# Performance work log

Measured on AMD Instinct MI355X. Metric: run time of the kernel, lower is better.

The kernel has to match this reference:

```python
import jax, jax.numpy as jnp
import numpy as np

BIG = 1e11  # torch code replaces zero counts with 1e11 before dividing
N_LABELS = 5


def _label_mean(state, func):
    """Masked mean per label (1..5). state [..., S, H], func [..., S] int.
    Returns aug [..., 5, H], aug_mask [..., 5] bool. Zero-count labels -> 0
    (sum is exactly 0 and denom is BIG, matching the torch zero-init path)."""
    mask = (func[..., None] == jnp.arange(1, N_LABELS + 1)).astype(state.dtype)  # [...,S,5]
    sums = jnp.einsum('...sl,...sh->...lh', mask, state)                          # [...,5,H]
    counts = mask.sum(axis=-2)                                                    # [...,5]
    aug_mask = counts > 0
    denom = jnp.where(aug_mask, counts, jnp.asarray(BIG, state.dtype))
    return sums / denom[..., None], aug_mask


def _masked_mean(state, func):
    """Mean over all non-pad (func != 0) sentences. state [..., S, H]."""
    m = (func != 0).astype(state.dtype)
    s = jnp.einsum('...s,...sh->...h', m, state)
    c = m.sum(axis=-1)
    pm = c > 0
    denom = jnp.where(pm, c, jnp.asarray(BIG, state.dtype))
    return s / denom[..., None], pm


def setup_inputs() -> dict:
    key = jax.random.key(0)
    k1, k2, k3, k4 = jax.random.split(key, 4)
    B, TS, H = 8, 512, 512       # batch, tar_n_sents, enc_hidden_size
    D, RS = 32, 256              # ref_n_docs, ref_n_sents
    return {
        'tarsent_state': jax.random.normal(k1, (B, TS, H), jnp.float32),
        'tar_func': jax.random.randint(k2, (B, TS), 0, 6),
        'refsent_state': jax.random.normal(k3, (B, D, RS, H), jnp.float32),
        'ref_func': jax.random.randint(k4, (B, D, RS), 0, 6),
    }


def reference(tarsent_state, tar_func, refsent_state, ref_func):
    # tar_aug_state [B,5,H], tar_aug_mask [B,5]
    tar_aug, tar_aug_mask = _label_mean(tarsent_state, tar_func)
    # ref_aug_state [B,D,5,H], ref_aug_mask [B,D,5]
    ref_aug, ref_aug_mask = _label_mean(refsent_state, ref_func)
    # tarpaper_state [B,H], refpaper_state [B,D,H]
    tarpaper_state, tar_mask2 = _masked_mean(tarsent_state, tar_func)
    refpaper_state, ref_mask2 = _masked_mean(refsent_state, ref_func)
    return (tar_aug, tar_aug_mask, ref_aug, ref_aug_mask,
            tarpaper_state, tar_mask2, refpaper_state, ref_mask2)
```

## Files before the change

### kernel.cpp

```cpp
#include <hip/hip_runtime.h>


#define H      512
#define HV     128
#define NL     5
#define BIGF   1e11f
#define CHUNK  64

#define OFF_TAR_AUG       0
#define OFF_TAR_AUG_MASK  20480
#define OFF_REF_AUG       20520
#define OFF_REF_AUG_MASK  675880
#define OFF_TARPAPER      677160
#define OFF_TAR_MASK2     681256
#define OFF_REFPAPER      681264
#define OFF_REF_MASK2     812336

#define NCHUNK_REF 4
#define NCHUNK_TAR 8
#define NBLK1      1088
#define WSUM_ELEMS ((size_t)NBLK1 * NL * H)
#define WCNT_OFF_B (WSUM_ELEMS * 4)
#define WS_NEED    (WCNT_OFF_B + (size_t)NBLK1 * NL * 4)

__device__ inline float4 f4add(float4 a, float4 b) {
    a.x += b.x; a.y += b.y; a.z += b.z; a.w += b.w; return a;
}
__device__ inline float4 f4scale(float4 a, float s) {
    a.x *= s; a.y *= s; a.z *= s; a.w *= s; return a;
}

__global__ __launch_bounds__(256) void emenc_stage1(
    const float* __restrict__ tar_state, const int* __restrict__ tar_func,
    const float* __restrict__ ref_state, const int* __restrict__ ref_func,
    float* __restrict__ wsum, int* __restrict__ wcnt)
{
    __shared__ int    sfunc[CHUNK];
    __shared__ float4 spart[HV * NL];
    __shared__ int    scnt[NL];

    const int b = blockIdx.x;
    const float* state;
    const int*   func;
    int s0;
    if (b < 1024) {
        const int seg = b >> 2, ch = b & 3;
        state = ref_state + (size_t)seg * 256 * H;
        func  = ref_func  + seg * 256;
        s0    = ch * CHUNK;
    } else {
        const int q = b - 1024;
        const int seg = q >> 3, ch = q & 7;
        state = tar_state + (size_t)seg * 512 * H;
        func  = tar_func  + seg * 512;
        s0    = ch * CHUNK;
    }

    const int tid = threadIdx.x;
    if (tid < CHUNK) sfunc[tid] = func[s0 + tid];
    __syncthreads();

    const int col   = tid & (HV - 1);
    const int phase = tid >> 7;

    float4 a1 = {0,0,0,0}, a2 = {0,0,0,0}, a3 = {0,0,0,0},
           a4 = {0,0,0,0}, a5 = {0,0,0,0};
    int c1 = 0, c2 = 0, c3 = 0, c4 = 0, c5 = 0;

    const float* base = state + (size_t)s0 * H;
    #pragma unroll 8
    for (int i = phase; i < CHUNK; i += 2) {
        float4 v = ((const float4*)(base + (size_t)i * H))[col];
        int l = sfunc[i];
        if      (l == 1) { a1 = f4add(a1, v); c1++; }
        else if (l == 2) { a2 = f4add(a2, v); c2++; }
        else if (l == 3) { a3 = f4add(a3, v); c3++; }
        else if (l == 4) { a4 = f4add(a4, v); c4++; }
        else if (l == 5) { a5 = f4add(a5, v); c5++; }
    }

    if (phase == 1) {
        spart[col * NL + 0] = a1;
        spart[col * NL + 1] = a2;
        spart[col * NL + 2] = a3;
        spart[col * NL + 3] = a4;
        spart[col * NL + 4] = a5;
        if (col == 0) {
            scnt[0] = c1; scnt[1] = c2; scnt[2] = c3; scnt[3] = c4; scnt[4] = c5;
        }
    }
    __syncthreads();

    if (phase == 0) {
        a1 = f4add(a1, spart[col * NL + 0]);
        a2 = f4add(a2, spart[col * NL + 1]);
        a3 = f4add(a3, spart[col * NL + 2]);
        a4 = f4add(a4, spart[col * NL + 3]);
        a5 = f4add(a5, spart[col * NL + 4]);

        float* wb = wsum + (size_t)b * NL * H;
        ((float4*)(wb + 0 * H))[col] = a1;
        ((float4*)(wb + 1 * H))[col] = a2;
        ((float4*)(wb + 2 * H))[col] = a3;
        ((float4*)(wb + 3 * H))[col] = a4;
        ((float4*)(wb + 4 * H))[col] = a5;

        if (col == 0) {
            wcnt[b * NL + 0] = c1 + scnt[0];
            wcnt[b * NL + 1] = c2 + scnt[1];
            wcnt[b * NL + 2] = c3 + scnt[2];
            wcnt[b * NL + 3] = c4 + scnt[3];
            wcnt[b * NL + 4] = c5 + scnt[4];
        }
    }
}

__global__ __launch_bounds__(128) void emenc_stage2(
    const float* __restrict__ wsum, const int* __restrict__ wcnt,
    float* __restrict__ out)
{
    __shared__ int scnt[NCHUNK_TAR * NL];

    const int b = blockIdx.x;
    int nch, wb0;
    float *aug, *augmask, *paper, *mask2;
    if (b < 256) {
        nch = NCHUNK_REF; wb0 = b * NCHUNK_REF;
        aug     = out + OFF_REF_AUG      + (size_t)b * NL * H;
        augmask = out + OFF_REF_AUG_MASK + b * NL;
        paper   = out + OFF_REFPAPER     + (size_t)b * H;
        mask2   = out + OFF_REF_MASK2    + b;
    } else {
        const int q = b - 256;
        nch = NCHUNK_TAR; wb0 = 1024 + q * NCHUNK_TAR;
        aug     = out + OFF_TAR_AUG      + (size_t)q * NL * H;
        augmask = out + OFF_TAR_AUG_MASK + q * NL;
        paper   = out + OFF_TARPAPER     + (size_t)q * H;
        mask2   = out + OFF_TAR_MASK2    + q;
    }

    const int tid = threadIdx.x;
    if (tid < nch * NL) scnt[tid] = wcnt[wb0 * NL + tid];
    __syncthreads();

    int c[NL], ct = 0;
    #pragma unroll
    for (int l = 0; l < NL; l++) {
        int s = 0;
        for (int ch = 0; ch < nch; ch++) s += scnt[ch * NL + l];
        c[l] = s; ct += s;
    }

    const int col = tid;
    float4 tot = {0,0,0,0};
    #pragma unroll
    for (int l = 0; l < NL; l++) {
        float4 s = {0,0,0,0};
        for (int ch = 0; ch < nch; ch++) {
            s = f4add(s, ((const float4*)(wsum + (size_t)(wb0 + ch) * NL * H
                                          + (size_t)l * H))[col]);
        }
        tot = f4add(tot, s);
        const float inv = 1.0f / (c[l] > 0 ? (float)c[l] : BIGF);
        ((float4*)(aug + (size_t)l * H))[col] = f4scale(s, inv);
    }
    ((float4*)paper)[col] = f4scale(tot, 1.0f / (ct > 0 ? (float)ct : BIGF));

    if (col == 0) {
        #pragma unroll
        for (int l = 0; l < NL; l++) augmask[l] = c[l] > 0 ? 1.0f : 0.0f;
        mask2[0] = ct > 0 ? 1.0f : 0.0f;
    }
}

__global__ __launch_bounds__(256) void emenc_single(
    const float* __restrict__ tar_state, const int* __restrict__ tar_func,
    const float* __restrict__ ref_state, const int* __restrict__ ref_func,
    float* __restrict__ out)
{
    __shared__ int    sfunc[512];
    __shared__ float4 spart[HV * NL];
    __shared__ int    scnt[NL];

    const int b = blockIdx.x;
    const float* state;
    const int*   func;
    int S;
    float *aug, *augmask, *paper, *mask2;

    if (b < 256) {
        state   = ref_state + (size_t)b * 256 * H;
        func    = ref_func  + b * 256;
        S       = 256;
        aug     = out + OFF_REF_AUG      + (size_t)b * NL * H;
        augmask = out + OFF_REF_AUG_MASK + b * NL;
        paper   = out + OFF_REFPAPER     + (size_t)b * H;
        mask2   = out + OFF_REF_MASK2    + b;
    } else {
        const int q = b - 256;
        state   = tar_state + (size_t)q * 512 * H;
        func    = tar_func  + q * 512;
        S       = 512;
        aug     = out + OFF_TAR_AUG      + (size_t)q * NL * H;
        augmask = out + OFF_TAR_AUG_MASK + q * NL;
        paper   = out + OFF_TARPAPER     + (size_t)q * H;
        mask2   = out + OFF_TAR_MASK2    + q;
    }

    const int tid = threadIdx.x;
    for (int i = tid; i < S; i += 256) sfunc[i] = func[i];
    __syncthreads();

    const int col   = tid & (HV - 1);
    const int phase = tid >> 7;

    float4 a1 = {0,0,0,0}, a2 = {0,0,0,0}, a3 = {0,0,0,0},
           a4 = {0,0,0,0}, a5 = {0,0,0,0};
    int c1 = 0, c2 = 0, c3 = 0, c4 = 0, c5 = 0;

    #pragma unroll 4
    for (int s = phase; s < S; s += 2) {
        float4 v = ((const float4*)(state + (size_t)s * H))[col];
        int l = sfunc[s];
        if      (l == 1) { a1 = f4add(a1, v); c1++; }
        else if (l == 2) { a2 = f4add(a2, v); c2++; }
        else if (l == 3) { a3 = f4add(a3, v); c3++; }
        else if (l == 4) { a4 = f4add(a4, v); c4++; }
        else if (l == 5) { a5 = f4add(a5, v); c5++; }
    }

    if (phase == 1) {
        spart[col * NL + 0] = a1;
        spart[col * NL + 1] = a2;
        spart[col * NL + 2] = a3;
        spart[col * NL + 3] = a4;
        spart[col * NL + 4] = a5;
        if (col == 0) {
            scnt[0] = c1; scnt[1] = c2; scnt[2] = c3; scnt[3] = c4; scnt[4] = c5;
        }
    }
    __syncthreads();

    if (phase == 0) {
        a1 = f4add(a1, spart[col * NL + 0]);
        a2 = f4add(a2, spart[col * NL + 1]);
        a3 = f4add(a3, spart[col * NL + 2]);
        a4 = f4add(a4, spart[col * NL + 3]);
        a5 = f4add(a5, spart[col * NL + 4]);
        c1 += scnt[0]; c2 += scnt[1]; c3 += scnt[2]; c4 += scnt[3]; c5 += scnt[4];

        float4 t  = f4add(f4add(f4add(a1, a2), f4add(a3, a4)), a5);
        const int ct = c1 + c2 + c3 + c4 + c5;

        ((float4*)(aug + 0 * H))[col] = f4scale(a1, 1.0f / (c1 > 0 ? (float)c1 : BIGF));
        ((float4*)(aug + 1 * H))[col] = f4scale(a2, 1.0f / (c2 > 0 ? (float)c2 : BIGF));
        ((float4*)(aug + 2 * H))[col] = f4scale(a3, 1.0f / (c3 > 0 ? (float)c3 : BIGF));
        ((float4*)(aug + 3 * H))[col] = f4scale(a4, 1.0f / (c4 > 0 ? (float)c4 : BIGF));
        ((float4*)(aug + 4 * H))[col] = f4scale(a5, 1.0f / (c5 > 0 ? (float)c5 : BIGF));
        ((float4*)paper)[col]         = f4scale(t,  1.0f / (ct > 0 ? (float)ct : BIGF));

        if (col == 0) {
            augmask[0] = c1 > 0 ? 1.0f : 0.0f;
            augmask[1] = c2 > 0 ? 1.0f : 0.0f;
            augmask[2] = c3 > 0 ? 1.0f : 0.0f;
            augmask[3] = c4 > 0 ? 1.0f : 0.0f;
            augmask[4] = c5 > 0 ? 1.0f : 0.0f;
            mask2[0]   = ct > 0 ? 1.0f : 0.0f;
        }
    }
}

extern "C" void kernel_launch(void* const* d_in, const int* in_sizes, int n_in,
                              void* d_out, int out_size, void* d_ws, size_t ws_size,
                              hipStream_t stream) {
    const float* tar_state = (const float*)d_in[0];
    const int*   tar_func  = (const int*)d_in[1];
    const float* ref_state = (const float*)d_in[2];
    const int*   ref_func  = (const int*)d_in[3];
    float* out = (float*)d_out;

    if (ws_size >= WS_NEED) {
        float* wsum = (float*)d_ws;
        int*   wcnt = (int*)((char*)d_ws + WCNT_OFF_B);
        emenc_stage1<<<NBLK1, 256, 0, stream>>>(tar_state, tar_func,
                                                ref_state, ref_func, wsum, wcnt);
        emenc_stage2<<<264, 128, 0, stream>>>(wsum, wcnt, out);
    } else {
        emenc_single<<<264, 256, 0, stream>>>(tar_state, tar_func,
                                              ref_state, ref_func, out);
    }
}
```

Baseline: 214.1 us.

## Halve stage1 chunk size and split stage2 work across six blocks per segment

Stage1 now processes 32-sentence chunks, doubling the block count to 2176 and fully unrolling the accumulation loop, so more loads are in flight. Stage2 launches six blocks per segment: one per label plus one for the paper mean. This spreads the reduction across many more CUs. In exchange the workspace partial sums double, so stage1 writes and stage2 reads twice as much intermediate data, and the paper-mean block re-reads all label partials.

```diff
diff --git a/kernel.cpp b/kernel.cpp
--- a/kernel.cpp
+++ b/kernel.cpp
@@ -5,7 +5,7 @@
 #define HV     128
 #define NL     5
 #define BIGF   1e11f
-#define CHUNK  64
+#define CHUNK  32
 
 #define OFF_TAR_AUG       0
 #define OFF_TAR_AUG_MASK  20480
@@ -16,9 +16,10 @@
 #define OFF_REFPAPER      681264
 #define OFF_REF_MASK2     812336
 
-#define NCHUNK_REF 4
-#define NCHUNK_TAR 8
-#define NBLK1      1088
+#define NCHUNK_REF 8
+#define NCHUNK_TAR 16
+#define NBLK_REF   2048
+#define NBLK1      2176
 #define WSUM_ELEMS ((size_t)NBLK1 * NL * H)
 #define WCNT_OFF_B (WSUM_ELEMS * 4)
 #define WS_NEED    (WCNT_OFF_B + (size_t)NBLK1 * NL * 4)
@@ -43,14 +44,14 @@
     const float* state;
     const int*   func;
     int s0;
-    if (b < 1024) {
-        const int seg = b >> 2, ch = b & 3;
+    if (b < NBLK_REF) {
+        const int seg = b >> 3, ch = b & 7;
         state = ref_state + (size_t)seg * 256 * H;
         func  = ref_func  + seg * 256;
         s0    = ch * CHUNK;
     } else {
-        const int q = b - 1024;
-        const int seg = q >> 3, ch = q & 7;
+        const int q = b - NBLK_REF;
+        const int seg = q >> 4, ch = q & 15;
         state = tar_state + (size_t)seg * 512 * H;
         func  = tar_func  + seg * 512;
         s0    = ch * CHUNK;
@@ -68,8 +69,9 @@
     int c1 = 0, c2 = 0, c3 = 0, c4 = 0, c5 = 0;
 
     const float* base = state + (size_t)s0 * H;
-    #pragma unroll 8
-    for (int i = phase; i < CHUNK; i += 2) {
+    #pragma unroll
+    for (int it = 0; it < CHUNK / 2; ++it) {
+        const int i = phase + 2 * it;
         float4 v = ((const float4*)(base + (size_t)i * H))[col];
         int l = sfunc[i];
         if      (l == 1) { a1 = f4add(a1, v); c1++; }
@@ -119,57 +121,53 @@
     const float* __restrict__ wsum, const int* __restrict__ wcnt,
     float* __restrict__ out)
 {
-    __shared__ int scnt[NCHUNK_TAR * NL];
-
-    const int b = blockIdx.x;
+    const int bb   = blockIdx.x;
+    const int seg  = bb / 6;
+    const int role = bb - seg * 6;
+
     int nch, wb0;
     float *aug, *augmask, *paper, *mask2;
-    if (b < 256) {
-        nch = NCHUNK_REF; wb0 = b * NCHUNK_REF;
-        aug     = out + OFF_REF_AUG      + (size_t)b * NL * H;
-        augmask = out + OFF_REF_AUG_MASK + b * NL;
-        paper   = out + OFF_REFPAPER     + (size_t)b * H;
-        mask2   = out + OFF_REF_MASK2    + b;
-    } else {
-        const int q = b - 256;
-        nch = NCHUNK_TAR; wb0 = 1024 + q * NCHUNK_TAR;
+    if (seg < 256) {
+        nch = NCHUNK_REF; wb0 = seg * NCHUNK_REF;
+        aug     = out + OFF_REF_AUG      + (size_t)seg * NL * H;
+        augmask = out + OFF_REF_AUG_MASK + seg * NL;
+        paper   = out + OFF_REFPAPER     + (size_t)seg * H;
+        mask2   = out + OFF_REF_MASK2    + seg;
+    } else {
+        const int q = seg - 256;
+        nch = NCHUNK_TAR; wb0 = NBLK_REF + q * NCHUNK_TAR;
         aug     = out + OFF_TAR_AUG      + (size_t)q * NL * H;
         augmask = out + OFF_TAR_AUG_MASK + q * NL;
         paper   = out + OFF_TARPAPER     + (size_t)q * H;
         mask2   = out + OFF_TAR_MASK2    + q;
     }
 
-    const int tid = threadIdx.x;
-    if (tid < nch * NL) scnt[tid] = wcnt[wb0 * NL + tid];
-    __syncthreads();
-
-    int c[NL], ct = 0;
-    #pragma unroll
-    for (int l = 0; l < NL; l++) {
-        int s = 0;
-        for (int ch = 0; ch < nch; ch++) s += scnt[ch * NL + l];
-        c[l] = s; ct += s;
-    }
-
-    const int col = tid;
-    float4 tot = {0,0,0,0};
-    #pragma unroll
-    for (int l = 0; l < NL; l++) {
+    const int col = threadIdx.x;
+
+    if (role < NL) {
+        int c = 0;
+        for (int ch = 0; ch < nch; ch++) c += wcnt[(wb0 + ch) * NL + role];
         float4 s = {0,0,0,0};
+        for (int ch = 0; ch < nch; ch++)
+            s = f4add(s, ((const float4*)(wsum + (size_t)(wb0 + ch) * NL * H
+                                          + (size_t)role * H))[col]);
+        const float inv = 1.0f / (c > 0 ? (float)c : BIGF);
+        ((float4*)(aug + (size_t)role * H))[col] = f4scale(s, inv);
+        if (col == 0) augmask[role] = c > 0 ? 1.0f : 0.0f;
+    } else {
+        int ct = 0;
         for (int ch = 0; ch < nch; ch++) {
-            s = f4add(s, ((const float4*)(wsum + (size_t)(wb0 + ch) * NL * H
-                                          + (size_t)l * H))[col]);
-        }
-        tot = f4add(tot, s);
-        const float inv = 1.0f / (c[l] > 0 ? (float)c[l] : BIGF);
-        ((float4*)(aug + (size_t)l * H))[col] = f4scale(s, inv);
-    }
-    ((float4*)paper)[col] = f4scale(tot, 1.0f / (ct > 0 ? (float)ct : BIGF));
-
-    if (col == 0) {
-        #pragma unroll
-        for (int l = 0; l < NL; l++) augmask[l] = c[l] > 0 ? 1.0f : 0.0f;
-        mask2[0] = ct > 0 ? 1.0f : 0.0f;
+            #pragma unroll
+            for (int l = 0; l < NL; l++) ct += wcnt[(wb0 + ch) * NL + l];
+        }
+        float4 t = {0,0,0,0};
+        for (int ch = 0; ch < nch; ch++) {
+            const float4* wb = (const float4*)(wsum + (size_t)(wb0 + ch) * NL * H);
+            #pragma unroll
+            for (int l = 0; l < NL; l++) t = f4add(t, wb[l * HV + col]);
+        }
+        ((float4*)paper)[col] = f4scale(t, 1.0f / (ct > 0 ? (float)ct : BIGF));
+        if (col == 0) mask2[0] = ct > 0 ? 1.0f : 0.0f;
     }
 }
 
@@ -284,7 +282,7 @@
         int*   wcnt = (int*)((char*)d_ws + WCNT_OFF_B);
         emenc_stage1<<<NBLK1, 256, 0, stream>>>(tar_state, tar_func,
                                                 ref_state, ref_func, wsum, wcnt);
-        emenc_stage2<<<264, 128, 0, stream>>>(wsum, wcnt, out);
+        emenc_stage2<<<264 * 6, 128, 0, stream>>>(wsum, wcnt, out);
     } else {
         emenc_single<<<264, 256, 0, stream>>>(tar_state, tar_func,
                                               ref_state, ref_func, out);
```

New measurement: 222.4 us. 1.04x slower.
